# Kernel optimization log

Hardware: AMD Instinct MI355X
Metric: run time of the kernel (lower is better)

Reference implementation:

```python
import jax, jax.numpy as jnp
import numpy as np

B, N, D = 4, 4096, 512      # batch, seq_len, model width
DIM_K = 64                   # per-head key dim used ONLY for the 1/sqrt scale
PROJ = 512                   # dim_k*heads = dim_v*heads = 64*8


def setup_inputs() -> dict:
    key = jax.random.key(0)
    ks = jax.random.split(key, 11)
    glorot = lambda k, shape: jax.random.uniform(
        k, shape, jnp.float32,
        -np.sqrt(6.0 / (shape[0] + shape[1])), np.sqrt(6.0 / (shape[0] + shape[1])))
    return {
        "q": jax.random.normal(ks[0], (B, N, D), jnp.float32),
        "k": jax.random.normal(ks[1], (B, N, D), jnp.float32),
        "v": jax.random.normal(ks[2], (B, N, D), jnp.float32),
        "w_q": glorot(ks[3], (D, PROJ)),
        "w_k": glorot(ks[4], (D, PROJ)),
        "w_v": glorot(ks[5], (D, PROJ)),
        "w_mha": glorot(ks[6], (PROJ, D)),
        "b_q": jnp.zeros((1, 1, PROJ), jnp.float32),
        "b_k": jnp.zeros((1, 1, PROJ), jnp.float32),
        "b_v": jnp.zeros((1, 1, PROJ), jnp.float32),
        "b_mha": jnp.zeros((1, 1, D), jnp.float32),
    }


def reference(q, k, v, w_q, w_k, w_v, w_mha, b_q, b_k, b_v, b_mha):
    # Projections (tensordot over last axis + broadcast bias)
    qp = jnp.einsum('bnd,de->bne', q, w_q) + b_q
    kp = jnp.einsum('bnd,de->bne', k, w_k) + b_k
    vp = jnp.einsum('bnd,de->bne', v, w_v) + b_v
    # NOTE: original call() forgets to pass heads=self.heads, so heads=1:
    # a single attention over the full PROJ width, scaled by sqrt(DIM_K).
    atts = jnp.einsum('bqe,bke->bqk', qp, kp) / np.sqrt(DIM_K).astype(np.float32)
    atts = jax.nn.softmax(atts, axis=-1)      # [B, N, N]
    dpa = jnp.einsum('bqk,bke->bqe', atts, vp)
    return jnp.einsum('bne,ed->bnd', dpa, w_mha) + b_mha
```

## Files before the change

kernel.cpp:

```cpp
#include <hip/hip_runtime.h>
#include <hip/hip_bf16.h>


typedef __attribute__((ext_vector_type(8))) short bf16x8;
typedef __attribute__((ext_vector_type(4))) float f32x4;

#define NB 4
#define NN 4096
#define ND 512

__device__ __forceinline__ f32x4 mfma16(bf16x8 a, bf16x8 b, f32x4 c) {
    return __builtin_amdgcn_mfma_f32_16x16x32_bf16(a, b, c, 0, 0, 0);
}
__device__ __forceinline__ short f2bf(float f) {
    __hip_bfloat16 h = __float2bfloat16(f);
    return *reinterpret_cast<short*>(&h);
}

typedef __attribute__((address_space(1))) const unsigned int gls_gt;
typedef __attribute__((address_space(3))) unsigned int gls_lt;
__device__ __forceinline__ void gll16(const void* g, void* l) {
    __builtin_amdgcn_global_load_lds((gls_gt*)g, (gls_lt*)l, 16, 0, 0);
}

struct Ptrs4 {
    const float* in[4];
    short* out[4];
};

__global__ void transpose_w(Ptrs4 p) {
    __shared__ short tile[32][33];
    const float* in = p.in[blockIdx.z];
    short* out = p.out[blockIdx.z];
    int r0 = blockIdx.y * 32, c0 = blockIdx.x * 32;
    int tx = threadIdx.x, ty = threadIdx.y;
    for (int i = 0; i < 32; i += 8)
        tile[ty + i][tx] = f2bf(in[(r0 + ty + i) * 512 + c0 + tx]);
    __syncthreads();
    for (int i = 0; i < 32; i += 8)
        out[(c0 + ty + i) * 512 + r0 + tx] = tile[tx][ty + i];
}

__global__ __launch_bounds__(256) void cast_f32_bf16(
    const float* __restrict__ in, short* __restrict__ out) {
    size_t i = (size_t)blockIdx.x * 256 + threadIdx.x;
    const float4* p = (const float4*)in + i * 2;
    float4 f0 = p[0], f1 = p[1];
    short tmp[8];
    tmp[0] = f2bf(f0.x); tmp[1] = f2bf(f0.y); tmp[2] = f2bf(f0.z); tmp[3] = f2bf(f0.w);
    tmp[4] = f2bf(f1.x); tmp[5] = f2bf(f1.y); tmp[6] = f2bf(f1.z); tmp[7] = f2bf(f1.w);
    *((bf16x8*)out + i) = *(bf16x8*)tmp;
}

template <int VT, int OF32>
__global__ __launch_bounds__(256, 4) void gemm_bt_bias(
    const short* __restrict__ A, const short* __restrict__ Bt,
    const float* __restrict__ bias, void* __restrict__ C) {
    __shared__ __align__(1024) char As[2 * 8192];
    __shared__ __align__(1024) char Bs[2 * 8192];
    int tid = threadIdx.x;
    int lane = tid & 63, w = tid >> 6;
    int l15 = lane & 15, l4 = lane >> 4;
    int wr = (w & 1) * 32, wcn = (w >> 1) * 32;
    int m0 = blockIdx.y * 64, n0 = blockIdx.x * 64;
    f32x4 acc[4] = {};

    int sr = lane >> 3;
    int sd = ((lane & 7) ^ sr) << 3;

#define STAGE_G(BUF, KT)                                                    \
    {                                                                       \
        _Pragma("unroll")                                                   \
        for (int i = 0; i < 2; i++) {                                       \
            int rbase = i * 32 + w * 8;                                     \
            gll16(&A[(size_t)(m0 + rbase + sr) * 512 + (KT) + sd],          \
                  As + (BUF) * 8192 + rbase * 128);                         \
            gll16(&Bt[(size_t)(n0 + rbase + sr) * 512 + (KT) + sd],         \
                  Bs + (BUF) * 8192 + rbase * 128);                         \
        }                                                                   \
    }

    STAGE_G(0, 0);
    for (int t = 0; t < 8; t++) {
        __syncthreads();
        if (t < 7) STAGE_G((t + 1) & 1, (t + 1) * 64);
        const char* Ab = As + (t & 1) * 8192;
        const char* Bb = Bs + (t & 1) * 8192;
#pragma unroll
        for (int kb = 0; kb < 2; kb++) {
            int ph = ((((kb << 2) | l4) ^ (l15 & 7)) << 4);
            bf16x8 a0 = *(const bf16x8*)(Ab + (wr + l15) * 128 + ph);
            bf16x8 a1 = *(const bf16x8*)(Ab + (wr + 16 + l15) * 128 + ph);
            bf16x8 b0 = *(const bf16x8*)(Bb + (wcn + l15) * 128 + ph);
            bf16x8 b1 = *(const bf16x8*)(Bb + (wcn + 16 + l15) * 128 + ph);
            acc[0] = mfma16(a0, b0, acc[0]);
            acc[1] = mfma16(a0, b1, acc[1]);
            acc[2] = mfma16(a1, b0, acc[2]);
            acc[3] = mfma16(a1, b1, acc[3]);
        }
    }
#undef STAGE_G
    for (int mi = 0; mi < 2; mi++)
        for (int ni = 0; ni < 2; ni++) {
            f32x4 vv = acc[mi * 2 + ni];
            int col = n0 + wcn + ni * 16 + l15;
            float bv = bias[col];
            for (int r = 0; r < 4; r++) {
                int row = m0 + wr + mi * 16 + l4 * 4 + r;
                float val = vv[r] + bv;
                if (VT) {
                    int b = row >> 12, j = row & 4095;
                    ((short*)C)[(size_t)b * (ND * NN) + (size_t)col * NN + j] = f2bf(val);
                } else if (OF32) {
                    ((float*)C)[(size_t)row * 512 + col] = val;
                } else {
                    ((short*)C)[(size_t)row * 512 + col] = f2bf(val);
                }
            }
        }
}

__global__ __launch_bounds__(512, 2) void flash_attn(
    const short* __restrict__ qp, const short* __restrict__ kp,
    const short* __restrict__ vpT, short* __restrict__ dpa) {
    __shared__ __align__(1024) char KsB[65536];
    __shared__ __align__(1024) char VsB[65536];
    __shared__ __align__(16)   char PldB[8192];
    __shared__ float SexM[128];
    __shared__ float SexS[128];

    int tid = threadIdx.x;
    int lane = tid & 63, w = tid >> 6;
    int l15 = lane & 15, l4 = lane >> 4;
    int wr = w & 3;
    int wc = w >> 2;
    int b = blockIdx.y;
    int q0 = blockIdx.x * 64;

    const short* qpb = qp + b * (NN * ND);
    const short* kpb = kp + b * (NN * ND);
    const short* vtb = vpT + b * (ND * NN);

    bf16x8 qf[16];
    {
        const short* qrow = qpb + (q0 + wr * 16 + l15) * ND + l4 * 8;
#pragma unroll
        for (int kb = 0; kb < 16; kb++) qf[kb] = *(const bf16x8*)(qrow + kb * 32);
    }
    f32x4 oacc[16] = {};
    float m_run[4], l_run[4];
#pragma unroll
    for (int r = 0; r < 4; r++) { m_run[r] = -1e30f; l_run[r] = 0.f; }

    const int vsl0 = ((l4 ^ (l15 & 7)) << 4);
    const int vsl1 = vsl0 ^ 64;

#define STAGE_K(J0)                                                         \
    {                                                                       \
        _Pragma("unroll")                                                   \
        for (int c = 0; c < 8; c++) {                                       \
            int key = w * 8 + c;                                            \
            const short* src = kpb + (size_t)((J0) + key) * ND +            \
                               ((lane ^ (key & 15)) << 3);                  \
            gll16(src, KsB + key * 1024);                                   \
        }                                                                   \
    }
#define STAGE_V(J0)                                                         \
    {                                                                       \
        _Pragma("unroll")                                                   \
        for (int c = 0; c < 8; c++) {                                       \
            int g = w * 8 + c;                                              \
            int e = g * 8 + (lane >> 3);                                    \
            const short* src = vtb + (size_t)e * NN + (J0) +                \
                               (((lane & 7) ^ (e & 7)) << 3);               \
            gll16(src, VsB + g * 1024);                                     \
        }                                                                   \
    }

    STAGE_K(0);
    STAGE_V(0);
    __syncthreads();

    for (int j0 = 0; j0 < NN; j0 += 64) {
        f32x4 s0 = {}, s1 = {};
        {
            const char* kb0 = KsB + (32 * wc + l15) * 1024;
            const char* kb1 = kb0 + 16 * 1024;
#pragma unroll
            for (int kb = 0; kb < 16; kb++) {
                int sl = ((((kb << 2) | l4) ^ l15) << 4);
                s0 = mfma16(qf[kb], *(const bf16x8*)(kb0 + sl), s0);
                s1 = mfma16(qf[kb], *(const bf16x8*)(kb1 + sl), s1);
            }
        }
        float vv0[4], vv1[4], mx[4], ss[4], p0[4], p1[4];
#pragma unroll
        for (int r = 0; r < 4; r++) {
            vv0[r] = s0[r] * 0.125f;
            vv1[r] = s1[r] * 0.125f;
            mx[r] = fmaxf(vv0[r], vv1[r]);
        }
#pragma unroll
        for (int off = 1; off <= 8; off <<= 1) {
#pragma unroll
            for (int r = 0; r < 4; r++) mx[r] = fmaxf(mx[r], __shfl_xor(mx[r], off));
        }
#pragma unroll
        for (int r = 0; r < 4; r++) {
            p0[r] = __expf(vv0[r] - mx[r]);
            p1[r] = __expf(vv1[r] - mx[r]);
            ss[r] = p0[r] + p1[r];
        }
#pragma unroll
        for (int off = 1; off <= 8; off <<= 1) {
#pragma unroll
            for (int r = 0; r < 4; r++) ss[r] += __shfl_xor(ss[r], off);
        }
        int row4 = wr * 16 + l4 * 4;
        if (l15 == 0) {
#pragma unroll
            for (int r = 0; r < 4; r++) {
                SexM[wc * 64 + row4 + r] = mx[r];
                SexS[wc * 64 + row4 + r] = ss[r];
            }
        }
        __syncthreads();
        float al4[4];
#pragma unroll
        for (int r = 0; r < 4; r++) {
            int row = row4 + r;
            float mo = SexM[(wc ^ 1) * 64 + row];
            float so = SexS[(wc ^ 1) * 64 + row];
            float mt = fmaxf(mx[r], mo);
            float st = ss[r] * __expf(mx[r] - mt) + so * __expf(mo - mt);
            float mn = fmaxf(m_run[r], mt);
            float al = __expf(m_run[r] - mn);
            l_run[r] = l_run[r] * al + st * __expf(mt - mn);
            m_run[r] = mn;
            al4[r] = al;
            float fs = __expf(mx[r] - mn);
            int rw7 = row & 7;
            char* prow = PldB + row * 128;
            int col0 = wc * 32 + l15;
            *(short*)(prow + (((col0 >> 3) ^ rw7) << 4) + ((col0 & 7) << 1)) = f2bf(p0[r] * fs);
            int col1 = col0 + 16;
            *(short*)(prow + (((col1 >> 3) ^ rw7) << 4) + ((col1 & 7) << 1)) = f2bf(p1[r] * fs);
        }
        {
            bool need = (al4[0] != 1.f) | (al4[1] != 1.f) |
                        (al4[2] != 1.f) | (al4[3] != 1.f);
            if (__any(need)) {
#pragma unroll
                for (int t = 0; t < 16; t++)
#pragma unroll
                    for (int r = 0; r < 4; r++) oacc[t][r] *= al4[r];
            }
        }
        __syncthreads();
        if (j0 + 64 < NN) STAGE_K(j0 + 64);
        bf16x8 pa0, pa1;
        {
            const char* prow = PldB + (wr * 16 + l15) * 128;
            pa0 = *(const bf16x8*)(prow + vsl0);
            pa1 = *(const bf16x8*)(prow + vsl1);
        }
#pragma unroll
        for (int eh = 0; eh < 2; eh++) {
#pragma unroll
            for (int i = 0; i < 8; i++) {
                const char* vb = VsB + (eh * 256 + 32 * i + 16 * wc + l15) * 128;
                int oi = eh * 8 + i;
                oacc[oi] = mfma16(pa0, *(const bf16x8*)(vb + vsl0), oacc[oi]);
                oacc[oi] = mfma16(pa1, *(const bf16x8*)(vb + vsl1), oacc[oi]);
            }
        }
        __syncthreads();
        if (j0 + 64 < NN) STAGE_V(j0 + 64);
    }
    float li[4];
#pragma unroll
    for (int r = 0; r < 4; r++) li[r] = 1.f / l_run[r];
    short* dpb = dpa + b * (NN * ND);
#pragma unroll
    for (int eh = 0; eh < 2; eh++)
#pragma unroll
        for (int i = 0; i < 8; i++) {
            int col = (16 * eh + 2 * i + wc) * 16 + l15;
#pragma unroll
            for (int r = 0; r < 4; r++) {
                int row = q0 + wr * 16 + l4 * 4 + r;
                dpb[row * ND + col] = f2bf(oacc[eh * 8 + i][r] * li[r]);
            }
        }
}

extern "C" void kernel_launch(void* const* d_in, const int* in_sizes, int n_in,
                              void* d_out, int out_size, void* d_ws, size_t ws_size,
                              hipStream_t stream) {
    const float* q     = (const float*)d_in[0];
    const float* k     = (const float*)d_in[1];
    const float* v     = (const float*)d_in[2];
    const float* w_q   = (const float*)d_in[3];
    const float* w_k   = (const float*)d_in[4];
    const float* w_v   = (const float*)d_in[5];
    const float* w_mha = (const float*)d_in[6];
    const float* b_q   = (const float*)d_in[7];
    const float* b_k   = (const float*)d_in[8];
    const float* b_v   = (const float*)d_in[9];
    const float* b_mha = (const float*)d_in[10];

    const size_t T = (size_t)NB * NN * ND;
    short* ws  = (short*)d_ws;
    short* qp  = ws;
    short* kp  = qp + T;
    short* vpT = kp + T;
    short* dpa = vpT + T;
    short* Wt  = dpa + T;

    Ptrs4 p;
    p.in[0] = w_q;   p.out[0] = Wt;
    p.in[1] = w_k;   p.out[1] = Wt + 262144;
    p.in[2] = w_v;   p.out[2] = Wt + 524288;
    p.in[3] = w_mha; p.out[3] = Wt + 786432;
    transpose_w<<<dim3(16, 16, 4), dim3(32, 8), 0, stream>>>(p);

    cast_f32_bf16<<<4096, 256, 0, stream>>>(q, dpa);
    gemm_bt_bias<0, 0><<<dim3(8, 256), 256, 0, stream>>>(dpa, Wt,          b_q, qp);
    cast_f32_bf16<<<4096, 256, 0, stream>>>(k, dpa);
    gemm_bt_bias<0, 0><<<dim3(8, 256), 256, 0, stream>>>(dpa, Wt + 262144, b_k, kp);
    cast_f32_bf16<<<4096, 256, 0, stream>>>(v, dpa);
    gemm_bt_bias<1, 0><<<dim3(8, 256), 256, 0, stream>>>(dpa, Wt + 524288, b_v, vpT);

    flash_attn<<<dim3(64, 4), 512, 0, stream>>>(qp, kp, vpT, dpa);

    gemm_bt_bias<0, 1><<<dim3(8, 256), 256, 0, stream>>>(dpa, Wt + 786432, b_mha, d_out);
}
```

Baseline: 538.4 us.

## Enlarge projection GEMM tiles to 128x128 and use DPP row reductions in softmax

The projection/output GEMM moves from 64x64 to 128x128 block tiles, with each wave computing a 64x64 sub-tile of 16 MFMA accumulators. This raises data reuse from LDS and cuts global traffic per FLOP, at the cost of more registers and LDS and fewer blocks. In the attention kernel, the 16-lane max and sum reductions switch from ds_swizzle/shuffle to DPP row_ror steps, which shortens the softmax critical path.

Result: faster. 471.7 us (-12.4%).

```diff
diff --git a/kernel.cpp b/kernel.cpp
--- a/kernel.cpp
+++ b/kernel.cpp
@@ -21,6 +21,28 @@
 typedef __attribute__((address_space(3))) unsigned int gls_lt;
 __device__ __forceinline__ void gll16(const void* g, void* l) {
     __builtin_amdgcn_global_load_lds((gls_gt*)g, (gls_lt*)l, 16, 0, 0);
+}
+
+#define DPP_ROR_STEP(V, CTRL, OP)                                              \
+    {                                                                          \
+        int _t = __builtin_amdgcn_update_dpp(0, __float_as_int(V), (CTRL),     \
+                                             0xf, 0xf, true);                  \
+        (V) = OP((V), __int_as_float(_t));                                     \
+    }
+__device__ __forceinline__ float faddf(float a, float b) { return a + b; }
+__device__ __forceinline__ float rmax16(float v) {
+    DPP_ROR_STEP(v, 0x128, fmaxf)
+    DPP_ROR_STEP(v, 0x124, fmaxf)
+    DPP_ROR_STEP(v, 0x122, fmaxf)
+    DPP_ROR_STEP(v, 0x121, fmaxf)
+    return v;
+}
+__device__ __forceinline__ float rsum16(float v) {
+    DPP_ROR_STEP(v, 0x128, faddf)
+    DPP_ROR_STEP(v, 0x124, faddf)
+    DPP_ROR_STEP(v, 0x122, faddf)
+    DPP_ROR_STEP(v, 0x121, faddf)
+    return v;
 }
 
 struct Ptrs4 {
@@ -53,17 +75,17 @@
 }
 
 template <int VT, int OF32>
-__global__ __launch_bounds__(256, 4) void gemm_bt_bias(
+__global__ __launch_bounds__(256, 2) void gemm_bt_bias(
     const short* __restrict__ A, const short* __restrict__ Bt,
     const float* __restrict__ bias, void* __restrict__ C) {
-    __shared__ __align__(1024) char As[2 * 8192];
-    __shared__ __align__(1024) char Bs[2 * 8192];
+    __shared__ __align__(1024) char As[2][16384];
+    __shared__ __align__(1024) char Bs[2][16384];
     int tid = threadIdx.x;
     int lane = tid & 63, w = tid >> 6;
     int l15 = lane & 15, l4 = lane >> 4;
-    int wr = (w & 1) * 32, wcn = (w >> 1) * 32;
-    int m0 = blockIdx.y * 64, n0 = blockIdx.x * 64;
-    f32x4 acc[4] = {};
+    int wr2 = (w & 1) * 64, wc2 = (w >> 1) * 64;
+    int m0 = blockIdx.y * 128, n0 = blockIdx.x * 128;
+    f32x4 acc[16] = {};
 
     int sr = lane >> 3;
     int sd = ((lane & 7) ^ sr) << 3;
@@ -71,12 +93,12 @@
 #define STAGE_G(BUF, KT)                                                    \
     {                                                                       \
         _Pragma("unroll")                                                   \
-        for (int i = 0; i < 2; i++) {                                       \
+        for (int i = 0; i < 4; i++) {                                       \
             int rbase = i * 32 + w * 8;                                     \
             gll16(&A[(size_t)(m0 + rbase + sr) * 512 + (KT) + sd],          \
-                  As + (BUF) * 8192 + rbase * 128);                         \
+                  As[BUF] + rbase * 128);                                   \
             gll16(&Bt[(size_t)(n0 + rbase + sr) * 512 + (KT) + sd],         \
-                  Bs + (BUF) * 8192 + rbase * 128);                         \
+                  Bs[BUF] + rbase * 128);                                   \
         }                                                                   \
     }
 
@@ -84,29 +106,33 @@
     for (int t = 0; t < 8; t++) {
         __syncthreads();
         if (t < 7) STAGE_G((t + 1) & 1, (t + 1) * 64);
-        const char* Ab = As + (t & 1) * 8192;
-        const char* Bb = Bs + (t & 1) * 8192;
+        const char* Ab = As[t & 1];
+        const char* Bb = Bs[t & 1];
 #pragma unroll
         for (int kb = 0; kb < 2; kb++) {
             int ph = ((((kb << 2) | l4) ^ (l15 & 7)) << 4);
-            bf16x8 a0 = *(const bf16x8*)(Ab + (wr + l15) * 128 + ph);
-            bf16x8 a1 = *(const bf16x8*)(Ab + (wr + 16 + l15) * 128 + ph);
-            bf16x8 b0 = *(const bf16x8*)(Bb + (wcn + l15) * 128 + ph);
-            bf16x8 b1 = *(const bf16x8*)(Bb + (wcn + 16 + l15) * 128 + ph);
-            acc[0] = mfma16(a0, b0, acc[0]);
-            acc[1] = mfma16(a0, b1, acc[1]);
-            acc[2] = mfma16(a1, b0, acc[2]);
-            acc[3] = mfma16(a1, b1, acc[3]);
+            bf16x8 af[4], bfr[4];
+#pragma unroll
+            for (int mi = 0; mi < 4; mi++)
+                af[mi] = *(const bf16x8*)(Ab + (wr2 + mi * 16 + l15) * 128 + ph);
+#pragma unroll
+            for (int ni = 0; ni < 4; ni++)
+                bfr[ni] = *(const bf16x8*)(Bb + (wc2 + ni * 16 + l15) * 128 + ph);
+#pragma unroll
+            for (int mi = 0; mi < 4; mi++)
+#pragma unroll
+                for (int ni = 0; ni < 4; ni++)
+                    acc[mi * 4 + ni] = mfma16(af[mi], bfr[ni], acc[mi * 4 + ni]);
         }
     }
 #undef STAGE_G
-    for (int mi = 0; mi < 2; mi++)
-        for (int ni = 0; ni < 2; ni++) {
-            f32x4 vv = acc[mi * 2 + ni];
-            int col = n0 + wcn + ni * 16 + l15;
+    for (int mi = 0; mi < 4; mi++)
+        for (int ni = 0; ni < 4; ni++) {
+            f32x4 vv = acc[mi * 4 + ni];
+            int col = n0 + wc2 + ni * 16 + l15;
             float bv = bias[col];
             for (int r = 0; r < 4; r++) {
-                int row = m0 + wr + mi * 16 + l4 * 4 + r;
+                int row = m0 + wr2 + mi * 16 + l4 * 4 + r;
                 float val = vv[r] + bv;
                 if (VT) {
                     int b = row >> 12, j = row & 4095;
@@ -198,23 +224,13 @@
         for (int r = 0; r < 4; r++) {
             vv0[r] = s0[r] * 0.125f;
             vv1[r] = s1[r] * 0.125f;
-            mx[r] = fmaxf(vv0[r], vv1[r]);
-        }
-#pragma unroll
-        for (int off = 1; off <= 8; off <<= 1) {
-#pragma unroll
-            for (int r = 0; r < 4; r++) mx[r] = fmaxf(mx[r], __shfl_xor(mx[r], off));
+            mx[r] = rmax16(fmaxf(vv0[r], vv1[r]));
         }
 #pragma unroll
         for (int r = 0; r < 4; r++) {
             p0[r] = __expf(vv0[r] - mx[r]);
             p1[r] = __expf(vv1[r] - mx[r]);
-            ss[r] = p0[r] + p1[r];
-        }
-#pragma unroll
-        for (int off = 1; off <= 8; off <<= 1) {
-#pragma unroll
-            for (int r = 0; r < 4; r++) ss[r] += __shfl_xor(ss[r], off);
+            ss[r] = rsum16(p0[r] + p1[r]);
         }
         int row4 = wr * 16 + l4 * 4;
         if (l15 == 0) {
@@ -325,13 +341,13 @@
     transpose_w<<<dim3(16, 16, 4), dim3(32, 8), 0, stream>>>(p);
 
     cast_f32_bf16<<<4096, 256, 0, stream>>>(q, dpa);
-    gemm_bt_bias<0, 0><<<dim3(8, 256), 256, 0, stream>>>(dpa, Wt,          b_q, qp);
+    gemm_bt_bias<0, 0><<<dim3(4, 128), 256, 0, stream>>>(dpa, Wt,          b_q, qp);
     cast_f32_bf16<<<4096, 256, 0, stream>>>(k, dpa);
-    gemm_bt_bias<0, 0><<<dim3(8, 256), 256, 0, stream>>>(dpa, Wt + 262144, b_k, kp);
+    gemm_bt_bias<0, 0><<<dim3(4, 128), 256, 0, stream>>>(dpa, Wt + 262144, b_k, kp);
     cast_f32_bf16<<<4096, 256, 0, stream>>>(v, dpa);
-    gemm_bt_bias<1, 0><<<dim3(8, 256), 256, 0, stream>>>(dpa, Wt + 524288, b_v, vpT);
+    gemm_bt_bias<1, 0><<<dim3(4, 128), 256, 0, stream>>>(dpa, Wt + 524288, b_v, vpT);
 
     flash_attn<<<dim3(64, 4), 512, 0, stream>>>(qp, kp, vpT, dpa);
 
-    gemm_bt_bias<0, 1><<<dim3(8, 256), 256, 0, stream>>>(dpa, Wt + 786432, b_mha, d_out);
-}
+    gemm_bt_bias<0, 1><<<dim3(4, 128), 256, 0, stream>>>(dpa, Wt + 786432, b_mha, d_out);
+}
```
